# Kernel optimization log

Measured on AMD Instinct MI355X. Metric: run time of the kernel, lower is better.

## Reference

```python
import jax, jax.numpy as jnp
import numpy as np

HIDDEN = 1024
D_FF = 2816
N_EXPERTS = 8
TOP_K = 2
TEMPERATURE = 1.0
LB_WEIGHT = 0.01


def setup_inputs() -> dict:
    key = jax.random.key(0)
    ks = jax.random.split(key, 5)
    scale_h = 1.0 / np.sqrt(HIDDEN)
    scale_f = 1.0 / np.sqrt(D_FF)
    x = jax.random.normal(ks[0], (2, 1024, HIDDEN), dtype=jnp.float32)
    gate_w = jax.random.normal(ks[1], (N_EXPERTS, HIDDEN), dtype=jnp.float32) * scale_h
    w1 = jax.random.normal(ks[2], (N_EXPERTS, HIDDEN, D_FF), dtype=jnp.float32) * scale_h  # gate proj
    w3 = jax.random.normal(ks[3], (N_EXPERTS, HIDDEN, D_FF), dtype=jnp.float32) * scale_h  # up proj
    w2 = jax.random.normal(ks[4], (N_EXPERTS, D_FF, HIDDEN), dtype=jnp.float32) * scale_f  # down proj
    return {"x": x, "gate_w": gate_w, "w1": w1, "w3": w3, "w2": w2}


def reference(x, gate_w, w1, w3, w2):
    B, S, H = x.shape
    xf = x.reshape(-1, H)                       # [T, H]
    T = xf.shape[0]

    # gating (eval mode: no routing noise)
    gate_logits = xf @ gate_w.T                 # [T, E]
    scaled = gate_logits / TEMPERATURE
    topk_vals, topk_idx = jax.lax.top_k(scaled, TOP_K)   # [T, K]
    topk_probs = jax.nn.softmax(topk_vals, axis=-1)      # [T, K]

    # dense combine weights: weight of expert e for token t (0 if not selected)
    onehot = jax.nn.one_hot(topk_idx, N_EXPERTS, dtype=xf.dtype)  # [T, K, E]
    comb = jnp.einsum("tke,tk->te", onehot, topk_probs)           # [T, E]

    # per-expert SwiGLU on all tokens, masked combine (math equals gather/scatter)
    h1 = jnp.einsum("th,ehf->etf", xf, w1)      # [E, T, F]
    h3 = jnp.einsum("th,ehf->etf", xf, w3)
    act = jax.nn.silu(h1) * h3                  # [E, T, F]
    y = jnp.einsum("etf,efh->eth", act, w2)     # [E, T, H]
    out = jnp.einsum("te,eth->th", comb, y)     # [T, H]

    # auxiliary load-balancing loss
    gate_probs = jax.nn.softmax(gate_logits, axis=-1)             # [T, E]
    expert_usage = onehot.sum(axis=(0, 1)) / (T * TOP_K + 1e-9)   # [E]
    gate_importance = gate_probs.mean(axis=0)                     # [E]
    aux = jnp.sum(expert_usage * gate_importance) * N_EXPERTS
    aux_loss = jnp.minimum(aux * LB_WEIGHT, 1.0)

    return out.reshape(B, S, H), aux_loss
```

## Files before the change

### kernel.cpp

```cpp
#include <hip/hip_runtime.h>
#include <hip/hip_bf16.h>
#include <math.h>


#define T_TOK 2048
#define HID   1024
#define DFF   2816
#define NE    8
#define ROWS  4096

typedef unsigned short u16;
typedef __attribute__((ext_vector_type(8))) short bf16x8;
typedef __attribute__((ext_vector_type(4))) float f32x4;

#define OFF_CNT    0
#define OFF_IMP    64
#define OFF_OFFS   128
#define OFF_TOPKI  256
#define OFF_TOPKP  (OFF_TOPKI + 16384)
#define OFF_BTOK   (OFF_TOPKP + 16384)
#define OFF_EPOS   (OFF_BTOK + 65536)
#define OFF_XB     (OFF_EPOS + 65536)
#define OFF_W1T    (OFF_XB + 4194304)
#define OFF_W3T    (OFF_W1T + 46137344)
#define OFF_W2T    (OFF_W3T + 46137344)
#define OFF_ACT    (OFF_W2T + 46137344)
#define WS_NEEDED  (OFF_ACT + 23068672)

__device__ __forceinline__ u16 f2bf(float f) {
    unsigned u = __float_as_uint(f);
    u = (u + 0x7fffu + ((u >> 16) & 1u)) >> 16;
    return (u16)u;
}

__device__ __forceinline__ void glds16(const void* g, void* l) {
    __builtin_amdgcn_global_load_lds(
        (const __attribute__((address_space(1))) unsigned int*)g,
        (__attribute__((address_space(3))) unsigned int*)l, 16, 0, 0);
}

__global__ void cvt_x_kernel(const float* __restrict__ x, u16* __restrict__ xb) {
    int i = blockIdx.x * 256 + threadIdx.x;
    float4 v = ((const float4*)x)[i];
    union { u16 s[4]; unsigned long long q; } o;
    o.s[0] = f2bf(v.x); o.s[1] = f2bf(v.y); o.s[2] = f2bf(v.z); o.s[3] = f2bf(v.w);
    ((unsigned long long*)xb)[i] = o.q;
}

__global__ void transpose_kernel(const float* __restrict__ in, u16* __restrict__ out,
                                 int K, int N) {
    __shared__ float tile[64][65];
    const float* ip = in + (size_t)blockIdx.z * K * N;
    u16* op = out + (size_t)blockIdx.z * K * N;
    int n0 = blockIdx.x * 64, k0 = blockIdx.y * 64;
    int tid = threadIdx.x;
#pragma unroll
    for (int p = 0; p < 4; ++p) {
        int row = p * 16 + (tid >> 4);
        int v = (tid & 15) * 4;
        float4 d = *(const float4*)(ip + (size_t)(k0 + row) * N + n0 + v);
        tile[row][v] = d.x; tile[row][v + 1] = d.y; tile[row][v + 2] = d.z; tile[row][v + 3] = d.w;
    }
    __syncthreads();
#pragma unroll
    for (int p = 0; p < 2; ++p) {
        int n = p * 32 + (tid >> 3);
        int g = (tid & 7) * 8;
        u16 o[8];
#pragma unroll
        for (int j = 0; j < 8; ++j) o[j] = f2bf(tile[g + j][n]);
        *(bf16x8*)(op + (size_t)(n0 + n) * K + k0 + g) = *(bf16x8*)o;
    }
}

__global__ void gating_kernel(const float* __restrict__ x, const float* __restrict__ gw,
                              int* __restrict__ topki, float* __restrict__ topkp,
                              float* __restrict__ imp) {
    __shared__ float s_imp[NE];
    int tid = threadIdx.x;
    if (tid < NE) s_imp[tid] = 0.f;
    __syncthreads();
    int lane = tid & 63;
    int t = blockIdx.x * 8 + (tid >> 6);
    float a[NE];
#pragma unroll
    for (int e = 0; e < NE; ++e) a[e] = 0.f;
#pragma unroll
    for (int c = 0; c < 16; ++c) {
        float xv = x[(size_t)t * HID + c * 64 + lane];
#pragma unroll
        for (int e = 0; e < NE; ++e) a[e] += xv * gw[e * HID + c * 64 + lane];
    }
#pragma unroll
    for (int e = 0; e < NE; ++e) {
#pragma unroll
        for (int off = 32; off > 0; off >>= 1) a[e] += __shfl_xor(a[e], off, 64);
    }
    if (lane == 0) {
        float v0 = -1e30f, v1 = -1e30f; int e0 = 0, e1 = 0;
#pragma unroll
        for (int e = 0; e < NE; ++e) {
            if (a[e] > v0) { v1 = v0; e1 = e0; v0 = a[e]; e0 = e; }
            else if (a[e] > v1) { v1 = a[e]; e1 = e; }
        }
        float p0 = 1.f / (1.f + expf(v1 - v0));
        topki[2 * t] = e0; topki[2 * t + 1] = e1;
        topkp[2 * t] = p0; topkp[2 * t + 1] = 1.f - p0;
        float s = 0.f, pe[NE];
#pragma unroll
        for (int e = 0; e < NE; ++e) { pe[e] = expf(a[e] - v0); s += pe[e]; }
        float inv = 1.f / s;
#pragma unroll
        for (int e = 0; e < NE; ++e) atomicAdd(&s_imp[e], pe[e] * inv);
    }
    __syncthreads();
    if (tid < NE) atomicAdd(&imp[tid], s_imp[tid]);
}

__global__ void compact_kernel(const int* __restrict__ topki,
                               int* __restrict__ cnt, int* __restrict__ btok,
                               int* __restrict__ epos) {
    int idx = blockIdx.x * 256 + threadIdx.x;
    int e = topki[idx];
    int pos = atomicAdd(&cnt[e], 1);
    btok[e * T_TOK + pos] = idx >> 1;
    epos[idx] = (e << 11) | pos;
}

__global__ void finalize_kernel(const int* __restrict__ cnt, const float* __restrict__ imp,
                                int* __restrict__ offs, float* __restrict__ aux_out) {
    if (threadIdx.x == 0) {
        int off = 0; float s = 0.f;
        for (int e = 0; e < NE; ++e) {
            offs[e] = off; off += cnt[e];
            s += ((float)cnt[e] / (4096.f + 1e-9f)) * (imp[e] / 2048.f);
        }
        aux_out[0] = fminf(s * 8.f * 0.01f, 1.f);
    }
}

__global__ __launch_bounds__(256, 3)
void gemm1_kernel(const u16* __restrict__ xb, const u16* __restrict__ w1t,
                  const u16* __restrict__ w3t, u16* __restrict__ act,
                  const int* __restrict__ btok, const int* __restrict__ cnt,
                  const int* __restrict__ offs) {
    int e = blockIdx.z;
    int n_e = cnt[e];
    int m0 = blockIdx.y * 128;
    if (m0 >= n_e) return;
    int nn0 = blockIdx.x * 64;
    int base = offs[e];

    __shared__ __align__(16) u16 As[2 * 128 * 32];
    __shared__ __align__(16) u16 B1s[2 * 64 * 32];
    __shared__ __align__(16) u16 B3s[2 * 64 * 32];

    int tid = threadIdx.x, lane = tid & 63, wv = tid >> 6;
    int wm = (wv >> 1) * 64, wn = (wv & 1) * 32;
    int l15 = lane & 15, quad = lane >> 4;

    int row0 = tid >> 2, row1 = 64 + row0;
    int q = (tid & 3) ^ ((tid >> 3) & 3);
    int sub = q * 8;
    int t0 = (m0 + row0 < n_e) ? btok[e * T_TOK + m0 + row0] : 0;
    int t1 = (m0 + row1 < n_e) ? btok[e * T_TOK + m0 + row1] : 0;
    const u16* ga0 = xb + (size_t)t0 * HID + sub;
    const u16* ga1 = xb + (size_t)t1 * HID + sub;
    const u16* g1 = w1t + ((size_t)e * DFF + nn0 + row0) * HID + sub;
    const u16* g3 = w3t + ((size_t)e * DFF + nn0 + row0) * HID + sub;
    int wa0 = (wv * 64) * 8;
    int wa1 = (256 + wv * 64) * 8;
    int wb  = (wv * 64) * 8;

    f32x4 acc1[4][2] = {}, acc3[4][2] = {};

    glds16(ga0, As + wa0); glds16(ga1, As + wa1);
    glds16(g1,  B1s + wb); glds16(g3,  B3s + wb);
    __syncthreads();

    int p = 0;
    for (int k0 = 0; k0 < HID; k0 += 32) {
        if (k0 + 32 < HID) {
            int nA = (p ^ 1) * 4096, nB = (p ^ 1) * 2048;
            glds16(ga0 + k0 + 32, As + nA + wa0); glds16(ga1 + k0 + 32, As + nA + wa1);
            glds16(g1 + k0 + 32, B1s + nB + wb);  glds16(g3 + k0 + 32, B3s + nB + wb);
        }
        const u16* Ab  = As  + p * 4096;
        const u16* B1b = B1s + p * 2048;
        const u16* B3b = B3s + p * 2048;
        bf16x8 af[4];
#pragma unroll
        for (int i = 0; i < 4; ++i) {
            int R = wm + i * 16 + l15;
            af[i] = *(const bf16x8*)&Ab[R * 32 + (quad ^ ((R >> 1) & 3)) * 8];
        }
#pragma unroll
        for (int j = 0; j < 2; ++j) {
            int R = wn + j * 16 + l15;
            int so = R * 32 + (quad ^ ((R >> 1) & 3)) * 8;
            bf16x8 b1 = *(const bf16x8*)&B1b[so];
            bf16x8 b3 = *(const bf16x8*)&B3b[so];
#pragma unroll
            for (int i = 0; i < 4; ++i) {
                acc1[i][j] = __builtin_amdgcn_mfma_f32_16x16x32_bf16(af[i], b1, acc1[i][j], 0, 0, 0);
                acc3[i][j] = __builtin_amdgcn_mfma_f32_16x16x32_bf16(af[i], b3, acc3[i][j], 0, 0, 0);
            }
        }
        __syncthreads();
        p ^= 1;
    }
#pragma unroll
    for (int i = 0; i < 4; ++i) {
#pragma unroll
        for (int r = 0; r < 4; ++r) {
            int m = m0 + wm + i * 16 + quad * 4 + r;
            if (m < n_e) {
#pragma unroll
                for (int j = 0; j < 2; ++j) {
                    float h1 = acc1[i][j][r], h3 = acc3[i][j][r];
                    float v = h1 / (1.f + expf(-h1)) * h3;
                    act[(size_t)(base + m) * DFF + nn0 + wn + j * 16 + l15] = f2bf(v);
                }
            }
        }
    }
}

__global__ __launch_bounds__(256, 3)
void gemm2_kernel(const u16* __restrict__ act, const u16* __restrict__ w2t,
                  float* __restrict__ ybuf, const int* __restrict__ cnt,
                  const int* __restrict__ offs) {
    int e = blockIdx.z;
    int n_e = cnt[e];
    int m0 = blockIdx.y * 64;
    if (m0 >= n_e) return;
    int nn0 = blockIdx.x * 128;
    int base = offs[e];

    __shared__ __align__(16) u16 As[2 * 2 * 64 * 32];
    __shared__ __align__(16) u16 Bs[2 * 2 * 128 * 32];

    int tid = threadIdx.x, lane = tid & 63, wv = tid >> 6;
    int wn = wv * 32;
    int l15 = lane & 15, quad = lane >> 4;

    int row0 = tid >> 2;
    int q = (tid & 3) ^ ((tid >> 3) & 3);
    int sub = q * 8;
    int ra = (m0 + row0 < n_e) ? (base + m0 + row0) : base;
    const u16* ga0 = act + (size_t)ra * DFF + sub;
    const u16* gb0 = w2t + ((size_t)e * HID + nn0 + row0) * DFF + sub;
    const u16* gb1 = w2t + ((size_t)e * HID + nn0 + 64 + row0) * DFF + sub;
    int wb = (wv * 64) * 8;

    f32x4 acc[4][2] = {};

#define STAGE2(P, K0)                                                          \
    do {                                                                       \
        _Pragma("unroll")                                                      \
        for (int h = 0; h < 2; ++h) {                                          \
            int ab = (P) * 4096 + h * 2048;                                    \
            int bb = (P) * 8192 + h * 4096;                                    \
            glds16(ga0 + (K0) + h * 32, As + ab + wb);                         \
            glds16(gb0 + (K0) + h * 32, Bs + bb + wb);                         \
            glds16(gb1 + (K0) + h * 32, Bs + bb + 2048 + wb);                  \
        }                                                                      \
    } while (0)

    STAGE2(0, 0);
    __syncthreads();

    int p = 0;
    for (int k0 = 0; k0 < DFF; k0 += 64) {
        if (k0 + 64 < DFF) STAGE2(p ^ 1, k0 + 64);
#pragma unroll
        for (int kk = 0; kk < 2; ++kk) {
            const u16* Ab = As + p * 4096 + kk * 2048;
            const u16* Bb = Bs + p * 8192 + kk * 4096;
            bf16x8 af[4];
#pragma unroll
            for (int i = 0; i < 4; ++i) {
                int R = i * 16 + l15;
                af[i] = *(const bf16x8*)&Ab[R * 32 + (quad ^ ((R >> 1) & 3)) * 8];
            }
#pragma unroll
            for (int j = 0; j < 2; ++j) {
                int R = wn + j * 16 + l15;
                bf16x8 bf = *(const bf16x8*)&Bb[R * 32 + (quad ^ ((R >> 1) & 3)) * 8];
#pragma unroll
                for (int i = 0; i < 4; ++i)
                    acc[i][j] = __builtin_amdgcn_mfma_f32_16x16x32_bf16(af[i], bf, acc[i][j], 0, 0, 0);
            }
        }
        __syncthreads();
        p ^= 1;
    }
#undef STAGE2
#pragma unroll
    for (int i = 0; i < 4; ++i) {
#pragma unroll
        for (int r = 0; r < 4; ++r) {
            int m = m0 + i * 16 + quad * 4 + r;
            if (m < n_e) {
#pragma unroll
                for (int j = 0; j < 2; ++j)
                    ybuf[(size_t)(base + m) * HID + nn0 + wn + j * 16 + l15] = acc[i][j][r];
            }
        }
    }
}

__global__ void combine_kernel(const float* __restrict__ ybuf, const int* __restrict__ epos,
                               const float* __restrict__ topkp, const int* __restrict__ offs,
                               float* __restrict__ out) {
    int t = blockIdx.x;
    int c = threadIdx.x * 4;
    int ep0 = epos[2 * t], ep1 = epos[2 * t + 1];
    int r0 = offs[ep0 >> 11] + (ep0 & 2047);
    int r1 = offs[ep1 >> 11] + (ep1 & 2047);
    float p0 = topkp[2 * t], p1 = topkp[2 * t + 1];
    float4 a = *(const float4*)&ybuf[(size_t)r0 * HID + c];
    float4 b = *(const float4*)&ybuf[(size_t)r1 * HID + c];
    float4 o;
    o.x = p0 * a.x + p1 * b.x; o.y = p0 * a.y + p1 * b.y;
    o.z = p0 * a.z + p1 * b.z; o.w = p0 * a.w + p1 * b.w;
    *(float4*)&out[(size_t)t * HID + c] = o;
}

extern "C" void kernel_launch(void* const* d_in, const int* in_sizes, int n_in,
                              void* d_out, int out_size, void* d_ws, size_t ws_size,
                              hipStream_t stream) {
    if (ws_size < (size_t)WS_NEEDED) return;

    const float* x  = (const float*)d_in[0];
    const float* gw = (const float*)d_in[1];
    const float* w1 = (const float*)d_in[2];
    const float* w3 = (const float*)d_in[3];
    const float* w2 = (const float*)d_in[4];
    float* out = (float*)d_out;

    char* ws = (char*)d_ws;
    int*   cnt   = (int*)(ws + OFF_CNT);
    float* imp   = (float*)(ws + OFF_IMP);
    int*   offs  = (int*)(ws + OFF_OFFS);
    int*   topki = (int*)(ws + OFF_TOPKI);
    float* topkp = (float*)(ws + OFF_TOPKP);
    int*   btok  = (int*)(ws + OFF_BTOK);
    int*   epos  = (int*)(ws + OFF_EPOS);
    u16*   xb    = (u16*)(ws + OFF_XB);
    u16*   w1t   = (u16*)(ws + OFF_W1T);
    u16*   w3t   = (u16*)(ws + OFF_W3T);
    u16*   w2t   = (u16*)(ws + OFF_W2T);
    u16*   actb  = (u16*)(ws + OFF_ACT);
    float* ybuf  = (float*)(ws + OFF_W1T);

    hipMemsetAsync(ws, 0, 256, stream);

    cvt_x_kernel<<<2048, 256, 0, stream>>>(x, xb);
    transpose_kernel<<<dim3(DFF / 64, HID / 64, NE), 256, 0, stream>>>(w1, w1t, HID, DFF);
    transpose_kernel<<<dim3(DFF / 64, HID / 64, NE), 256, 0, stream>>>(w3, w3t, HID, DFF);
    transpose_kernel<<<dim3(HID / 64, DFF / 64, NE), 256, 0, stream>>>(w2, w2t, DFF, HID);

    gating_kernel<<<T_TOK / 8, 512, 0, stream>>>(x, gw, topki, topkp, imp);
    compact_kernel<<<ROWS / 256, 256, 0, stream>>>(topki, cnt, btok, epos);
    finalize_kernel<<<1, 64, 0, stream>>>(cnt, imp, offs, out + (size_t)T_TOK * HID);

    gemm1_kernel<<<dim3(DFF / 64, T_TOK / 128, NE), 256, 0, stream>>>(
        xb, w1t, w3t, actb, btok, cnt, offs);
    gemm2_kernel<<<dim3(HID / 128, T_TOK / 64, NE), 256, 0, stream>>>(
        actb, w2t, ybuf, cnt, offs);
    combine_kernel<<<T_TOK, 256, 0, stream>>>(ybuf, epos, topkp, offs, out);
}
```

Measured before the change: 471.6 us.

## Merge prep kernels into one launch and deepen gemm1 LDS prefetch pipeline

Fuses x conversion, three weight transposes and gating into a single prep kernel that dispatches on block index, which removes several launches and the gaps between them. The gemm1 main loop now issues global-to-LDS loads two stages ahead, using explicit vmcnt waits and raw barriers in place of __syncthreads, so loads overlap more with MFMA work. The hand-counted vmcnt and barrier placement is fragile, and the larger fused kernel may use more registers or lose occupancy in some branches.

```diff
diff --git a/kernel.cpp b/kernel.cpp
--- a/kernel.cpp
+++ b/kernel.cpp
@@ -27,6 +27,12 @@
 #define OFF_ACT    (OFF_W2T + 46137344)
 #define WS_NEEDED  (OFF_ACT + 23068672)
 
+#define PB_W1   5632
+#define PB_W3   11264
+#define PB_W2   16896
+#define PB_CVT  18944
+#define PB_GATE 19456
+
 __device__ __forceinline__ u16 f2bf(float f) {
     unsigned u = __float_as_uint(f);
     u = (u + 0x7fffu + ((u >> 16) & 1u)) >> 16;
@@ -39,21 +45,9 @@
         (__attribute__((address_space(3))) unsigned int*)l, 16, 0, 0);
 }
 
-__global__ void cvt_x_kernel(const float* __restrict__ x, u16* __restrict__ xb) {
-    int i = blockIdx.x * 256 + threadIdx.x;
-    float4 v = ((const float4*)x)[i];
-    union { u16 s[4]; unsigned long long q; } o;
-    o.s[0] = f2bf(v.x); o.s[1] = f2bf(v.y); o.s[2] = f2bf(v.z); o.s[3] = f2bf(v.w);
-    ((unsigned long long*)xb)[i] = o.q;
-}
-
-__global__ void transpose_kernel(const float* __restrict__ in, u16* __restrict__ out,
-                                 int K, int N) {
-    __shared__ float tile[64][65];
-    const float* ip = in + (size_t)blockIdx.z * K * N;
-    u16* op = out + (size_t)blockIdx.z * K * N;
-    int n0 = blockIdx.x * 64, k0 = blockIdx.y * 64;
-    int tid = threadIdx.x;
+__device__ __forceinline__ void transpose_body(const float* ip, u16* op, int K, int N,
+                                               int n0, int k0, int tid,
+                                               float tile[64][65]) {
 #pragma unroll
     for (int p = 0; p < 4; ++p) {
         int row = p * 16 + (tid >> 4);
@@ -73,48 +67,75 @@
     }
 }
 
-__global__ void gating_kernel(const float* __restrict__ x, const float* __restrict__ gw,
-                              int* __restrict__ topki, float* __restrict__ topkp,
-                              float* __restrict__ imp) {
+__global__ void prep_kernel(const float* __restrict__ x, u16* __restrict__ xb,
+                            const float* __restrict__ w1, u16* __restrict__ w1t,
+                            const float* __restrict__ w3, u16* __restrict__ w3t,
+                            const float* __restrict__ w2, u16* __restrict__ w2t,
+                            const float* __restrict__ gw, int* __restrict__ topki,
+                            float* __restrict__ topkp, float* __restrict__ imp) {
+    __shared__ float tile[64][65];
     __shared__ float s_imp[NE];
-    int tid = threadIdx.x;
-    if (tid < NE) s_imp[tid] = 0.f;
-    __syncthreads();
-    int lane = tid & 63;
-    int t = blockIdx.x * 8 + (tid >> 6);
-    float a[NE];
-#pragma unroll
-    for (int e = 0; e < NE; ++e) a[e] = 0.f;
-#pragma unroll
-    for (int c = 0; c < 16; ++c) {
-        float xv = x[(size_t)t * HID + c * 64 + lane];
-#pragma unroll
-        for (int e = 0; e < NE; ++e) a[e] += xv * gw[e * HID + c * 64 + lane];
-    }
-#pragma unroll
-    for (int e = 0; e < NE; ++e) {
-#pragma unroll
-        for (int off = 32; off > 0; off >>= 1) a[e] += __shfl_xor(a[e], off, 64);
-    }
-    if (lane == 0) {
-        float v0 = -1e30f, v1 = -1e30f; int e0 = 0, e1 = 0;
+    int id = blockIdx.x, tid = threadIdx.x;
+
+    if (id < PB_W3) {
+        const float* in = (id < PB_W1) ? w1 : w3;
+        u16* out = (id < PB_W1) ? w1t : w3t;
+        int id1 = (id < PB_W1) ? id : id - PB_W1;
+        int bx = id1 % 44, byz = id1 / 44;
+        int by = byz & 15, bz = byz >> 4;
+        transpose_body(in + (size_t)bz * HID * DFF, out + (size_t)bz * HID * DFF,
+                       HID, DFF, bx * 64, by * 64, tid, tile);
+    } else if (id < PB_W2) {
+        int id2 = id - PB_W3;
+        int bx = id2 & 15, byz = id2 >> 4;
+        int by = byz % 44, bz = byz / 44;
+        transpose_body(w2 + (size_t)bz * DFF * HID, w2t + (size_t)bz * DFF * HID,
+                       DFF, HID, bx * 64, by * 64, tid, tile);
+    } else if (id < PB_CVT) {
+        int i = (id - PB_W2) * 256 + tid;
+        float4 v = ((const float4*)x)[i];
+        union { u16 s[4]; unsigned long long q; } o;
+        o.s[0] = f2bf(v.x); o.s[1] = f2bf(v.y); o.s[2] = f2bf(v.z); o.s[3] = f2bf(v.w);
+        ((unsigned long long*)xb)[i] = o.q;
+    } else {
+        if (tid < NE) s_imp[tid] = 0.f;
+        __syncthreads();
+        int lane = tid & 63;
+        int t = (id - PB_CVT) * 4 + (tid >> 6);
+        float a[NE];
+#pragma unroll
+        for (int e = 0; e < NE; ++e) a[e] = 0.f;
+#pragma unroll
+        for (int c = 0; c < 16; ++c) {
+            float xv = x[(size_t)t * HID + c * 64 + lane];
+#pragma unroll
+            for (int e = 0; e < NE; ++e) a[e] += xv * gw[e * HID + c * 64 + lane];
+        }
 #pragma unroll
         for (int e = 0; e < NE; ++e) {
-            if (a[e] > v0) { v1 = v0; e1 = e0; v0 = a[e]; e0 = e; }
-            else if (a[e] > v1) { v1 = a[e]; e1 = e; }
-        }
-        float p0 = 1.f / (1.f + expf(v1 - v0));
-        topki[2 * t] = e0; topki[2 * t + 1] = e1;
-        topkp[2 * t] = p0; topkp[2 * t + 1] = 1.f - p0;
-        float s = 0.f, pe[NE];
-#pragma unroll
-        for (int e = 0; e < NE; ++e) { pe[e] = expf(a[e] - v0); s += pe[e]; }
-        float inv = 1.f / s;
-#pragma unroll
-        for (int e = 0; e < NE; ++e) atomicAdd(&s_imp[e], pe[e] * inv);
-    }
-    __syncthreads();
-    if (tid < NE) atomicAdd(&imp[tid], s_imp[tid]);
+#pragma unroll
+            for (int off = 32; off > 0; off >>= 1) a[e] += __shfl_xor(a[e], off, 64);
+        }
+        if (lane == 0) {
+            float v0 = -1e30f, v1 = -1e30f; int e0 = 0, e1 = 0;
+#pragma unroll
+            for (int e = 0; e < NE; ++e) {
+                if (a[e] > v0) { v1 = v0; e1 = e0; v0 = a[e]; e0 = e; }
+                else if (a[e] > v1) { v1 = a[e]; e1 = e; }
+            }
+            float p0 = 1.f / (1.f + expf(v1 - v0));
+            topki[2 * t] = e0; topki[2 * t + 1] = e1;
+            topkp[2 * t] = p0; topkp[2 * t + 1] = 1.f - p0;
+            float s = 0.f, pe[NE];
+#pragma unroll
+            for (int e = 0; e < NE; ++e) { pe[e] = expf(a[e] - v0); s += pe[e]; }
+            float inv = 1.f / s;
+#pragma unroll
+            for (int e = 0; e < NE; ++e) atomicAdd(&s_imp[e], pe[e] * inv);
+        }
+        __syncthreads();
+        if (tid < NE) atomicAdd(&imp[tid], s_imp[tid]);
+    }
 }
 
 __global__ void compact_kernel(const int* __restrict__ topki,
@@ -168,23 +189,27 @@
     const u16* ga1 = xb + (size_t)t1 * HID + sub;
     const u16* g1 = w1t + ((size_t)e * DFF + nn0 + row0) * HID + sub;
     const u16* g3 = w3t + ((size_t)e * DFF + nn0 + row0) * HID + sub;
-    int wa0 = (wv * 64) * 8;
-    int wa1 = (256 + wv * 64) * 8;
-    int wb  = (wv * 64) * 8;
+    int wa0 = wv * 512;
+    int wa1 = 2048 + wv * 512;
+    int wb  = wv * 512;
 
     f32x4 acc1[4][2] = {}, acc3[4][2] = {};
 
-    glds16(ga0, As + wa0); glds16(ga1, As + wa1);
-    glds16(g1,  B1s + wb); glds16(g3,  B3s + wb);
-    __syncthreads();
+#define STG1(BUF, K0) do {                                                     \
+        int nA_ = (BUF) * 4096, nB_ = (BUF) * 2048;                            \
+        glds16(ga0 + (K0), As + nA_ + wa0); glds16(ga1 + (K0), As + nA_ + wa1);\
+        glds16(g1 + (K0), B1s + nB_ + wb);  glds16(g3 + (K0), B3s + nB_ + wb); \
+    } while (0)
+
+    STG1(0, 0);
+    STG1(1, 32);
 
     int p = 0;
     for (int k0 = 0; k0 < HID; k0 += 32) {
-        if (k0 + 32 < HID) {
-            int nA = (p ^ 1) * 4096, nB = (p ^ 1) * 2048;
-            glds16(ga0 + k0 + 32, As + nA + wa0); glds16(ga1 + k0 + 32, As + nA + wa1);
-            glds16(g1 + k0 + 32, B1s + nB + wb);  glds16(g3 + k0 + 32, B3s + nB + wb);
-        }
+        if (k0 + 32 < HID) asm volatile("s_waitcnt vmcnt(4)" ::: "memory");
+        else               asm volatile("s_waitcnt vmcnt(0)" ::: "memory");
+        __builtin_amdgcn_s_barrier();
+        asm volatile("" ::: "memory");
         const u16* Ab  = As  + p * 4096;
         const u16* B1b = B1s + p * 2048;
         const u16* B3b = B3s + p * 2048;
@@ -206,9 +231,13 @@
                 acc3[i][j] = __builtin_amdgcn_mfma_f32_16x16x32_bf16(af[i], b3, acc3[i][j], 0, 0, 0);
             }
         }
-        __syncthreads();
+        asm volatile("" ::: "memory");
+        __builtin_amdgcn_s_barrier();
+        asm volatile("" ::: "memory");
+        if (k0 + 64 < HID) STG1(p, k0 + 64);
         p ^= 1;
     }
+#undef STG1
 #pragma unroll
     for (int i = 0; i < 4; ++i) {
 #pragma unroll
@@ -356,12 +385,8 @@
 
     hipMemsetAsync(ws, 0, 256, stream);
 
-    cvt_x_kernel<<<2048, 256, 0, stream>>>(x, xb);
-    transpose_kernel<<<dim3(DFF / 64, HID / 64, NE), 256, 0, stream>>>(w1, w1t, HID, DFF);
-    transpose_kernel<<<dim3(DFF / 64, HID / 64, NE), 256, 0, stream>>>(w3, w3t, HID, DFF);
-    transpose_kernel<<<dim3(HID / 64, DFF / 64, NE), 256, 0, stream>>>(w2, w2t, DFF, HID);
-
-    gating_kernel<<<T_TOK / 8, 512, 0, stream>>>(x, gw, topki, topkp, imp);
+    prep_kernel<<<PB_GATE, 256, 0, stream>>>(x, xb, w1, w1t, w3, w3t, w2, w2t,
+                                             gw, topki, topkp, imp);
     compact_kernel<<<ROWS / 256, 256, 0, stream>>>(topki, cnt, btok, epos);
     finalize_kernel<<<1, 64, 0, stream>>>(cnt, imp, offs, out + (size_t)T_TOK * HID);
 
```

Result: faster. 454.2 us (-3.7%).
